# Performance work log

Hardware: AMD Instinct MI355X
Metric: run time of the kernel (lower is better)

Reference implementation:

```python
import jax, jax.numpy as jnp
import numpy as np

N = 50000      # num_nodes
E = 800000     # num_edges
F = 29         # num_node_features
IN = F + 3     # in_channels after hstack with pos
H = 64         # hidden_dim
B = 50         # batch_size (num graphs)
L = 7          # num GINConv layers


def setup_inputs() -> dict:
    key = jax.random.key(0)
    ks = jax.random.split(key, 12)
    s_in = 1.0 / np.sqrt(IN)
    s_h = 1.0 / np.sqrt(H)
    return {
        "x": jax.random.normal(ks[0], (N, F), jnp.float32),
        "pos": jax.random.normal(ks[1], (N, 3), jnp.float32),
        "edge_index": jax.random.randint(ks[2], (2, E), 0, N),
        "batch": jnp.sort(jax.random.randint(ks[3], (N,), 0, B)),
        # GINConv l: MLP = Linear(in,H) -> ReLU -> Linear(H,H)
        "W1_first": jax.random.normal(ks[4], (IN, H), jnp.float32) * s_in,
        "W1_rest": jax.random.normal(ks[5], (L - 1, H, H), jnp.float32) * s_h,
        "b1": jax.random.normal(ks[6], (L, H), jnp.float32) * 0.01,
        "W2": jax.random.normal(ks[7], (L, H, H), jnp.float32) * s_h,
        "b2": jax.random.normal(ks[8], (L, H), jnp.float32) * 0.01,
        "lin_w": jax.random.normal(ks[9], (H, 1), jnp.float32) * s_h,
        "lin_b": jax.random.normal(ks[10], (1,), jnp.float32) * 0.01,
    }


def reference(x, pos, edge_index, batch, W1_first, W1_rest, b1, W2, b2, lin_w, lin_b):
    src, dst = edge_index[0], edge_index[1]
    h = jnp.concatenate([x, pos], axis=1)  # [N, IN]

    def gin_conv(h, Wa, ba, Wb, bb):
        # sum aggregation of source features at destination nodes, eps=0
        agg = jax.ops.segment_sum(h[src], dst, num_segments=N)
        z = h + agg
        z = jax.nn.relu(z @ Wa + ba)
        return z @ Wb + bb

    h = jax.nn.relu(gin_conv(h, W1_first, b1[0], W2[0], b2[0]))
    for l in range(1, L):
        h = gin_conv(h, W1_rest[l - 1], b1[l], W2[l], b2[l])
        if l < L - 1:  # no activation after last conv (jk=None)
            h = jax.nn.relu(h)

    # global mean pool per graph
    sums = jax.ops.segment_sum(h, batch, num_segments=B)            # [B, H]
    counts = jax.ops.segment_sum(jnp.ones((N,), h.dtype), batch, num_segments=B)
    pooled = sums / jnp.maximum(counts, 1.0)[:, None]

    return pooled @ lin_w + lin_b  # [B, 1]
```

## Files before the change

kernel.cpp:

```cpp
#include <hip/hip_runtime.h>
#include <stdint.h>

#define NF 29
#define HD 64
#define NL 7
#define LDW 72
#define NCHUNK 256
#define BSH 8
#define PER_M (64 * LDW)

typedef __attribute__((ext_vector_type(8))) __bf16 bf16x8;
typedef __attribute__((ext_vector_type(4))) float floatx4;

__device__ __forceinline__ unsigned short f2bf(float x) {
    unsigned u = __float_as_uint(x);
    unsigned r = (u + 0x7fffu + ((u >> 16) & 1u)) >> 16;
    return (unsigned short)r;
}
__device__ __forceinline__ unsigned pack_bf2(float x, float y) {
    return (unsigned)f2bf(x) | ((unsigned)f2bf(y) << 16);
}
__device__ __forceinline__ float bflo(uint32_t u) { return __uint_as_float(u << 16); }
__device__ __forceinline__ float bfhi(uint32_t u) { return __uint_as_float(u & 0xffff0000u); }

__global__ void init_kernel(const float* __restrict__ x, const float* __restrict__ pos,
                            unsigned short* __restrict__ h0,
                            const float* __restrict__ W1f, const float* __restrict__ W1r,
                            const float* __restrict__ W2, unsigned short* __restrict__ wpk,
                            int N) {
    int t = blockIdx.x * blockDim.x + threadIdx.x;
    if (t < NL * 2 * PER_M) {
        int l = t / (2 * PER_M);
        int r = t - l * 2 * PER_M;
        int m = r / PER_M;
        int q = r - m * PER_M;
        int j = q / LDW, k = q - j * LDW;
        float v = 0.f;
        if (m == 0) {
            int ind = (l == 0) ? 32 : 64;
            if (k < ind) v = (l == 0) ? W1f[k * 64 + j]
                                      : W1r[(size_t)(l - 1) * 4096 + (size_t)k * 64 + j];
        } else {
            if (k < 64) v = W2[(size_t)l * 4096 + (size_t)k * 64 + j];
        }
        wpk[t] = f2bf(v);
    }
    if (t < N * 32) {
        int n = t >> 5, f = t & 31;
        float v = (f < NF) ? x[n * NF + f] : pos[n * 3 + (f - NF)];
        h0[t] = f2bf(v);
    }
}

__global__ void bucket_hist_kernel(const int* __restrict__ dst, int E, int chunk,
                                   int* __restrict__ bcnt, int* __restrict__ bsum) {
    __shared__ int hist[256];
    int tid = threadIdx.x;
    hist[tid] = 0;
    __syncthreads();
    int lo = blockIdx.x * chunk, hi = min(E, lo + chunk);
    for (int e = lo + tid; e < hi; e += 256) atomicAdd(&hist[dst[e] >> BSH], 1);
    __syncthreads();
    bcnt[tid * NCHUNK + blockIdx.x] = hist[tid];
    if (hist[tid]) atomicAdd(&bsum[tid], hist[tid]);
}

__global__ void bstart_scan_kernel(const int* __restrict__ bsum, int* __restrict__ bstart,
                                   int* __restrict__ rowptr, int nbuk, int N, int E) {
    __shared__ int s[256];
    int t = threadIdx.x;
    s[t] = (t < nbuk) ? bsum[t] : 0;
    __syncthreads();
    for (int off = 1; off < 256; off <<= 1) {
        int v = (t >= off) ? s[t - off] : 0;
        __syncthreads();
        s[t] += v;
        __syncthreads();
    }
    bstart[t] = (t == 0) ? 0 : s[t - 1];
    if (t == 255) bstart[256] = s[255];
    if (t == 0) rowptr[N] = E;
}

__global__ void bucket_off_kernel(const int* __restrict__ bcnt, const int* __restrict__ bstart,
                                  int* __restrict__ boffT) {
    __shared__ int s[256];
    int b = blockIdx.x, t = threadIdx.x;
    int c = bcnt[b * NCHUNK + t];
    s[t] = c;
    __syncthreads();
    for (int off = 1; off < 256; off <<= 1) {
        int v = (t >= off) ? s[t - off] : 0;
        __syncthreads();
        s[t] += v;
        __syncthreads();
    }
    int excl = s[t] - c;
    boffT[t * 256 + b] = bstart[b] + excl;
}

__global__ void bucket_scatter_kernel(const int* __restrict__ src, const int* __restrict__ dst,
                                      int E, int chunk, const int* __restrict__ boffT,
                                      unsigned int* __restrict__ ebuf) {
    __shared__ int cur[256];
    int tid = threadIdx.x, c = blockIdx.x;
    cur[tid] = boffT[c * 256 + tid];
    __syncthreads();
    int lo = c * chunk, hi = min(E, lo + chunk);
    for (int e = lo + tid; e < hi; e += 256) {
        int d = dst[e];
        int p = atomicAdd(&cur[d >> BSH], 1);
        ebuf[p] = (unsigned int)src[e] | ((unsigned int)(d & 255) << 16);
    }
}

__global__ void final_scatter_kernel(const unsigned int* __restrict__ ebuf,
                                     const int* __restrict__ bstart,
                                     int* __restrict__ rowptr,
                                     unsigned short* __restrict__ colsrc, int N) {
    __shared__ int cnt[256];
    __shared__ int cur[256];
    __shared__ int s[256];
    int b = blockIdx.x, t = threadIdx.x;
    cnt[t] = 0;
    __syncthreads();
    int lo = bstart[b], hi = bstart[b + 1];
    for (int e = lo + t; e < hi; e += 256) atomicAdd(&cnt[ebuf[e] >> 16], 1);
    __syncthreads();
    int c = cnt[t];
    s[t] = c;
    __syncthreads();
    for (int off = 1; off < 256; off <<= 1) {
        int v = (t >= off) ? s[t - off] : 0;
        __syncthreads();
        s[t] += v;
        __syncthreads();
    }
    int base = lo + s[t] - c;
    int node = (b << BSH) + t;
    if (node < N) rowptr[node] = base;
    cur[t] = base;
    __syncthreads();
    for (int e = lo + t; e < hi; e += 256) {
        unsigned int ed = ebuf[e];
        int p = atomicAdd(&cur[ed >> 16], 1);
        colsrc[p] = (unsigned short)(ed & 0xffffu);
    }
}

template<int IND, bool RELU_OUT>
__global__ __launch_bounds__(512, 8)
void gin_layer_kernel(const unsigned short* __restrict__ hin,
                      const int* __restrict__ rowptr, const unsigned short* __restrict__ colsrc,
                      const unsigned short* __restrict__ wAT, const unsigned short* __restrict__ wBT,
                      const float* __restrict__ ba, const float* __restrict__ bb,
                      unsigned short* __restrict__ hout, int N)
{
    __shared__ __align__(16) unsigned short zbuf[64 * LDW];
    __shared__ __align__(16) unsigned short t1buf[64 * LDW];

    const int tid = threadIdx.x;
    const int lane = tid & 63;
    const int w = tid >> 6;
    const int tile0 = blockIdx.x * 64;

    const uint4* hin4 = (const uint4*)hin;
    const int g = lane >> 3;
    const int j = lane & 7;
    const int node = tile0 + w * 8 + g;

    int rp;
    {
        int idx = tile0 + w * 8 + (lane < 9 ? lane : 8);
        if (idx > N) idx = N;
        rp = rowptr[idx];
    }
    int e0 = __shfl(rp, g);
    int e1 = __shfl(rp, g + 1);
    if (node >= N) { e0 = 0; e1 = 0; }

    float acc[8] = {0.f, 0.f, 0.f, 0.f, 0.f, 0.f, 0.f, 0.f};
    auto addrow = [&](uint4 u) {
        acc[0] += bflo(u.x); acc[1] += bfhi(u.x);
        acc[2] += bflo(u.y); acc[3] += bfhi(u.y);
        acc[4] += bflo(u.z); acc[5] += bfhi(u.z);
        acc[6] += bflo(u.w); acc[7] += bfhi(u.w);
    };

    if constexpr (IND == 64) {
        const int f4 = lane & 7;
        if (node < N) addrow(hin4[(size_t)node * 8 + f4]);
        int e = e0;
        int idxv = (e + j < e1) ? (int)colsrc[e + j] : 0;
        for (; e + 7 < e1; e += 8) {
            int en = e + 8;
            int idx_next = (en + j < e1) ? (int)colsrc[en + j] : 0;
            int s[8];
            #pragma unroll
            for (int q = 0; q < 8; ++q) s[q] = __shfl(idxv, g * 8 + q);
            uint4 u[8];
            #pragma unroll
            for (int q = 0; q < 8; ++q) u[q] = hin4[(size_t)s[q] * 8 + f4];
            #pragma unroll
            for (int q = 0; q < 8; ++q) addrow(u[q]);
            idxv = idx_next;
        }
        {
            int rem = e1 - e;
            #pragma unroll
            for (int q = 0; q < 8; ++q) {
                if (q < rem) {
                    int s = __shfl(idxv, g * 8 + q);
                    addrow(hin4[(size_t)s * 8 + f4]);
                }
            }
        }
        uint4 pk;
        pk.x = pack_bf2(acc[0], acc[1]); pk.y = pack_bf2(acc[2], acc[3]);
        pk.z = pack_bf2(acc[4], acc[5]); pk.w = pack_bf2(acc[6], acc[7]);
        *(uint4*)&zbuf[(w * 8 + g) * LDW + f4 * 8] = pk;
    } else {
        const int p = (lane >> 2) & 1;
        const int f4 = lane & 3;
        if (node < N && p == 0) addrow(hin4[(size_t)node * 4 + f4]);
        int e = e0 + p;
        for (; e + 7 < e1; e += 8) {
            int s0 = colsrc[e], s1 = colsrc[e + 2], s2 = colsrc[e + 4], s3 = colsrc[e + 6];
            uint4 u0 = hin4[(size_t)s0 * 4 + f4];
            uint4 u1 = hin4[(size_t)s1 * 4 + f4];
            uint4 u2 = hin4[(size_t)s2 * 4 + f4];
            uint4 u3 = hin4[(size_t)s3 * 4 + f4];
            addrow(u0); addrow(u1); addrow(u2); addrow(u3);
        }
        while (e < e1) { addrow(hin4[(size_t)colsrc[e] * 4 + f4]); e += 2; }
        #pragma unroll
        for (int i = 0; i < 8; ++i) acc[i] += __shfl_xor(acc[i], 4);
        if (p == 0) {
            uint4 pk;
            pk.x = pack_bf2(acc[0], acc[1]); pk.y = pack_bf2(acc[2], acc[3]);
            pk.z = pack_bf2(acc[4], acc[5]); pk.w = pack_bf2(acc[6], acc[7]);
            *(uint4*)&zbuf[(w * 8 + g) * LDW + f4 * 8] = pk;
        }
    }
    __syncthreads();

    const int n0 = lane & 15, quad = lane >> 4;
    const int stripe = w & 3, jhalf = w >> 2;
    const int row0 = stripe * 16;
    const int jt0 = jhalf * 2, jt1 = jhalf * 2 + 1;

    floatx4 c0, c1;
    {
        float b0v = ba[jt0 * 16 + n0], b1v = ba[jt1 * 16 + n0];
        c0 = (floatx4){b0v, b0v, b0v, b0v};
        c1 = (floatx4){b1v, b1v, b1v, b1v};
    }
    #pragma unroll
    for (int kk = 0; kk < IND / 32; ++kk) {
        bf16x8 a   = *(const bf16x8*)&zbuf[(row0 + n0) * LDW + kk * 32 + quad * 8];
        bf16x8 br0 = *(const bf16x8*)&wAT[(jt0 * 16 + n0) * LDW + kk * 32 + quad * 8];
        bf16x8 br1 = *(const bf16x8*)&wAT[(jt1 * 16 + n0) * LDW + kk * 32 + quad * 8];
        c0 = __builtin_amdgcn_mfma_f32_16x16x32_bf16(a, br0, c0, 0, 0, 0);
        c1 = __builtin_amdgcn_mfma_f32_16x16x32_bf16(a, br1, c1, 0, 0, 0);
    }
    #pragma unroll
    for (int r = 0; r < 4; ++r) {
        int row = row0 + quad * 4 + r;
        t1buf[row * LDW + jt0 * 16 + n0] = f2bf(fmaxf(c0[r], 0.f));
        t1buf[row * LDW + jt1 * 16 + n0] = f2bf(fmaxf(c1[r], 0.f));
    }
    __syncthreads();

    {
        float b0v = bb[jt0 * 16 + n0], b1v = bb[jt1 * 16 + n0];
        c0 = (floatx4){b0v, b0v, b0v, b0v};
        c1 = (floatx4){b1v, b1v, b1v, b1v};
    }
    #pragma unroll
    for (int kk = 0; kk < 2; ++kk) {
        bf16x8 a   = *(const bf16x8*)&t1buf[(row0 + n0) * LDW + kk * 32 + quad * 8];
        bf16x8 br0 = *(const bf16x8*)&wBT[(jt0 * 16 + n0) * LDW + kk * 32 + quad * 8];
        bf16x8 br1 = *(const bf16x8*)&wBT[(jt1 * 16 + n0) * LDW + kk * 32 + quad * 8];
        c0 = __builtin_amdgcn_mfma_f32_16x16x32_bf16(a, br0, c0, 0, 0, 0);
        c1 = __builtin_amdgcn_mfma_f32_16x16x32_bf16(a, br1, c1, 0, 0, 0);
    }
    #pragma unroll
    for (int r = 0; r < 4; ++r) {
        int row = row0 + quad * 4 + r;
        float v0 = c0[r], v1 = c1[r];
        if (RELU_OUT) { v0 = fmaxf(v0, 0.f); v1 = fmaxf(v1, 0.f); }
        zbuf[row * LDW + jt0 * 16 + n0] = f2bf(v0);
        zbuf[row * LDW + jt1 * 16 + n0] = f2bf(v1);
    }
    __syncthreads();

    {
        int nl = tid >> 3, c4 = tid & 7;
        int nodeo = tile0 + nl;
        if (nodeo < N) {
            uint4 v = *(const uint4*)&zbuf[nl * LDW + c4 * 8];
            ((uint4*)hout)[(size_t)nodeo * 8 + c4] = v;
        }
    }
}

__global__ void pool_kernel(const unsigned short* __restrict__ h, const int* __restrict__ batch,
                            float* __restrict__ pool, float* __restrict__ cnt, int N) {
    int lane = threadIdx.x;
    int nblk = gridDim.x;
    int per = (N + nblk - 1) / nblk;
    int lo = blockIdx.x * per, hi = min(N, lo + per);
    if (lo >= hi) return;
    int cur = batch[lo];
    float acc = 0.f, c = 0.f;
    for (int n = lo; n < hi; ++n) {
        int b = batch[n];
        if (b != cur) {
            atomicAdd(&pool[cur * HD + lane], acc);
            if (lane == 0) atomicAdd(&cnt[cur], c);
            acc = 0.f; c = 0.f; cur = b;
        }
        acc += __uint_as_float((uint32_t)h[(size_t)n * HD + lane] << 16);
        c += 1.f;
    }
    atomicAdd(&pool[cur * HD + lane], acc);
    if (lane == 0) atomicAdd(&cnt[cur], c);
}

__global__ void final_kernel(const float* __restrict__ pool, const float* __restrict__ cnt,
                             const float* __restrict__ lin_w, const float* __restrict__ lin_b,
                             float* __restrict__ out, int B) {
    int b = blockIdx.x;
    int lane = threadIdx.x;
    float c = fmaxf(cnt[b], 1.f);
    float v = pool[b * HD + lane] / c * lin_w[lane];
    for (int off = 32; off > 0; off >>= 1) v += __shfl_down(v, off);
    if (lane == 0) out[b] = v + lin_b[0];
}

extern "C" void kernel_launch(void* const* d_in, const int* in_sizes, int n_in,
                              void* d_out, int out_size, void* d_ws, size_t ws_size,
                              hipStream_t stream)
{
    const float* x   = (const float*)d_in[0];
    const float* pos = (const float*)d_in[1];
    const int*  eidx = (const int*)d_in[2];
    const int* batch = (const int*)d_in[3];
    const float* W1f = (const float*)d_in[4];
    const float* W1r = (const float*)d_in[5];
    const float* b1  = (const float*)d_in[6];
    const float* W2  = (const float*)d_in[7];
    const float* b2  = (const float*)d_in[8];
    const float* lw  = (const float*)d_in[9];
    const float* lb  = (const float*)d_in[10];

    int N = in_sizes[3];
    int E = in_sizes[2] / 2;
    int B = out_size;
    const int* src = eidx;
    const int* dst = eidx + E;

    char* ws = (char*)d_ws;
    size_t off = 0;
    auto alloc = [&](size_t bytes) -> void* {
        void* p = ws + off;
        off += (bytes + 255) & ~(size_t)255;
        return p;
    };
    unsigned short* bufA = (unsigned short*)alloc((size_t)N * HD * 2);
    unsigned short* bufB = (unsigned short*)alloc((size_t)N * HD * 2);
    int*   rowptr = (int*)  alloc((size_t)(N + 1) * 4);
    unsigned short* colsrc = (unsigned short*)alloc((size_t)E * 2);
    unsigned int* ebuf = (unsigned int*)alloc((size_t)E * 4);
    float* pool   = (float*)alloc((size_t)B * HD * 4);
    float* cnt    = (float*)alloc((size_t)B * 4);
    int*   bcnt   = (int*)  alloc((size_t)256 * NCHUNK * 4);
    int*   boffT  = (int*)  alloc((size_t)NCHUNK * 256 * 4);
    int*   bsum   = (int*)  alloc(256 * 4);
    int*   bstart = (int*)  alloc(257 * 4);
    unsigned short* wpk = (unsigned short*)alloc((size_t)NL * 2 * PER_M * 2);

    hipMemsetAsync(bsum, 0, 256 * 4, stream);
    hipMemsetAsync(pool, 0, (size_t)B * HD * 4, stream);
    hipMemsetAsync(cnt, 0, (size_t)B * 4, stream);

    int nbuk = (N + 255) >> BSH;
    int chunk = (E + NCHUNK - 1) / NCHUNK;

    init_kernel<<<(N * 32 + 255) / 256, 256, 0, stream>>>(x, pos, bufA, W1f, W1r, W2, wpk, N);
    bucket_hist_kernel<<<NCHUNK, 256, 0, stream>>>(dst, E, chunk, bcnt, bsum);
    bstart_scan_kernel<<<1, 256, 0, stream>>>(bsum, bstart, rowptr, nbuk, N, E);
    bucket_off_kernel<<<nbuk, 256, 0, stream>>>(bcnt, bstart, boffT);
    bucket_scatter_kernel<<<NCHUNK, 256, 0, stream>>>(src, dst, E, chunk, boffT, ebuf);
    final_scatter_kernel<<<nbuk, 256, 0, stream>>>(ebuf, bstart, rowptr, colsrc, N);

    const int gblocks = (N + 63) / 64;
    gin_layer_kernel<32, true><<<gblocks, 512, 0, stream>>>(
        bufA, rowptr, colsrc, wpk + 0 * PER_M, wpk + 1 * PER_M, b1, b2, bufB, N);
    unsigned short* cur_in = bufB;
    unsigned short* cur_out = bufA;
    for (int l = 1; l < NL; ++l) {
        const unsigned short* wa = wpk + (size_t)(2 * l + 0) * PER_M;
        const unsigned short* wb = wpk + (size_t)(2 * l + 1) * PER_M;
        const float* ba = b1 + l * HD;
        const float* bb = b2 + l * HD;
        if (l < NL - 1)
            gin_layer_kernel<HD, true><<<gblocks, 512, 0, stream>>>(
                cur_in, rowptr, colsrc, wa, wb, ba, bb, cur_out, N);
        else
            gin_layer_kernel<HD, false><<<gblocks, 512, 0, stream>>>(
                cur_in, rowptr, colsrc, wa, wb, ba, bb, cur_out, N);
        unsigned short* tmp = cur_in; cur_in = cur_out; cur_out = tmp;
    }
    pool_kernel<<<512, 64, 0, stream>>>(cur_in, batch, pool, cnt, N);
    final_kernel<<<B, 64, 0, stream>>>(pool, cnt, lw, lb, (float*)d_out, B);
}
```

Baseline: 291.8 us.

## Split 64-wide node features into two 32-wide halves gathered in separate passes

Stores hidden features as two separate 32-column bf16 tables. Each layer now runs a gather kernel for the low half into a staging buffer, then the fused layer kernel gathers the high half and does the MLP. The aim is to shrink each random-gather working set (1.6MB per half) so it fits better in cache and gets higher hit rates. In exchange it adds an extra kernel launch per layer, a round trip of the low-half aggregate through global memory, and a second walk of the edge list.

Measured after the change: 322.4 us. +10.5%, slower.

```diff
diff --git a/kernel.cpp b/kernel.cpp
--- a/kernel.cpp
+++ b/kernel.cpp
@@ -148,98 +148,116 @@
     }
 }
 
-template<int IND, bool RELU_OUT>
-__global__ __launch_bounds__(512, 8)
-void gin_layer_kernel(const unsigned short* __restrict__ hin,
-                      const int* __restrict__ rowptr, const unsigned short* __restrict__ colsrc,
-                      const unsigned short* __restrict__ wAT, const unsigned short* __restrict__ wBT,
-                      const float* __restrict__ ba, const float* __restrict__ bb,
-                      unsigned short* __restrict__ hout, int N)
-{
-    __shared__ __align__(16) unsigned short zbuf[64 * LDW];
-    __shared__ __align__(16) unsigned short t1buf[64 * LDW];
-
-    const int tid = threadIdx.x;
-    const int lane = tid & 63;
-    const int w = tid >> 6;
-    const int tile0 = blockIdx.x * 64;
-
-    const uint4* hin4 = (const uint4*)hin;
-    const int g = lane >> 3;
-    const int j = lane & 7;
-    const int node = tile0 + w * 8 + g;
-
-    int rp;
-    {
-        int idx = tile0 + w * 8 + (lane < 9 ? lane : 8);
-        if (idx > N) idx = N;
-        rp = rowptr[idx];
-    }
-    int e0 = __shfl(rp, g);
-    int e1 = __shfl(rp, g + 1);
-    if (node >= N) { e0 = 0; e1 = 0; }
-
-    float acc[8] = {0.f, 0.f, 0.f, 0.f, 0.f, 0.f, 0.f, 0.f};
+template<bool SELF>
+__device__ __forceinline__ void gather32(const uint4* __restrict__ tab4,
+                                         const unsigned short* __restrict__ colsrc,
+                                         int node, int e0, int e1, int lane,
+                                         float acc[8]) {
+    const int p = (lane >> 2) & 1;
+    const int f4 = lane & 3;
     auto addrow = [&](uint4 u) {
         acc[0] += bflo(u.x); acc[1] += bfhi(u.x);
         acc[2] += bflo(u.y); acc[3] += bfhi(u.y);
         acc[4] += bflo(u.z); acc[5] += bfhi(u.z);
         acc[6] += bflo(u.w); acc[7] += bfhi(u.w);
     };
-
-    if constexpr (IND == 64) {
-        const int f4 = lane & 7;
-        if (node < N) addrow(hin4[(size_t)node * 8 + f4]);
-        int e = e0;
-        int idxv = (e + j < e1) ? (int)colsrc[e + j] : 0;
-        for (; e + 7 < e1; e += 8) {
-            int en = e + 8;
-            int idx_next = (en + j < e1) ? (int)colsrc[en + j] : 0;
-            int s[8];
-            #pragma unroll
-            for (int q = 0; q < 8; ++q) s[q] = __shfl(idxv, g * 8 + q);
-            uint4 u[8];
-            #pragma unroll
-            for (int q = 0; q < 8; ++q) u[q] = hin4[(size_t)s[q] * 8 + f4];
-            #pragma unroll
-            for (int q = 0; q < 8; ++q) addrow(u[q]);
-            idxv = idx_next;
-        }
-        {
-            int rem = e1 - e;
-            #pragma unroll
-            for (int q = 0; q < 8; ++q) {
-                if (q < rem) {
-                    int s = __shfl(idxv, g * 8 + q);
-                    addrow(hin4[(size_t)s * 8 + f4]);
-                }
-            }
-        }
+    if (SELF && node >= 0 && p == 0) addrow(tab4[(size_t)node * 4 + f4]);
+    int e = e0 + p;
+    for (; e + 7 < e1; e += 8) {
+        int s0 = colsrc[e], s1 = colsrc[e + 2], s2 = colsrc[e + 4], s3 = colsrc[e + 6];
+        uint4 u0 = tab4[(size_t)s0 * 4 + f4];
+        uint4 u1 = tab4[(size_t)s1 * 4 + f4];
+        uint4 u2 = tab4[(size_t)s2 * 4 + f4];
+        uint4 u3 = tab4[(size_t)s3 * 4 + f4];
+        addrow(u0); addrow(u1); addrow(u2); addrow(u3);
+    }
+    while (e < e1) { addrow(tab4[(size_t)colsrc[e] * 4 + f4]); e += 2; }
+    #pragma unroll
+    for (int i = 0; i < 8; ++i) acc[i] += __shfl_xor(acc[i], 4);
+}
+
+__global__ __launch_bounds__(512, 8)
+void gather_lo_kernel(const unsigned short* __restrict__ hA,
+                      const int* __restrict__ rowptr, const unsigned short* __restrict__ colsrc,
+                      unsigned short* __restrict__ zlo, int N)
+{
+    const int tid = threadIdx.x;
+    const int lane = tid & 63;
+    const int w = tid >> 6;
+    const int tile0 = blockIdx.x * 64;
+    const int g = lane >> 3;
+    const int node = tile0 + w * 8 + g;
+
+    int rp;
+    {
+        int idx = tile0 + w * 8 + (lane < 9 ? lane : 8);
+        if (idx > N) idx = N;
+        rp = rowptr[idx];
+    }
+    int e0 = __shfl(rp, g);
+    int e1 = __shfl(rp, g + 1);
+    bool valid = (node < N);
+    if (!valid) { e0 = 0; e1 = 0; }
+
+    float acc[8] = {0.f, 0.f, 0.f, 0.f, 0.f, 0.f, 0.f, 0.f};
+    gather32<true>((const uint4*)hA, colsrc, valid ? node : -1, e0, e1, lane, acc);
+
+    if (valid && ((lane >> 2) & 1) == 0) {
         uint4 pk;
         pk.x = pack_bf2(acc[0], acc[1]); pk.y = pack_bf2(acc[2], acc[3]);
         pk.z = pack_bf2(acc[4], acc[5]); pk.w = pack_bf2(acc[6], acc[7]);
-        *(uint4*)&zbuf[(w * 8 + g) * LDW + f4 * 8] = pk;
-    } else {
-        const int p = (lane >> 2) & 1;
-        const int f4 = lane & 3;
-        if (node < N && p == 0) addrow(hin4[(size_t)node * 4 + f4]);
-        int e = e0 + p;
-        for (; e + 7 < e1; e += 8) {
-            int s0 = colsrc[e], s1 = colsrc[e + 2], s2 = colsrc[e + 4], s3 = colsrc[e + 6];
-            uint4 u0 = hin4[(size_t)s0 * 4 + f4];
-            uint4 u1 = hin4[(size_t)s1 * 4 + f4];
-            uint4 u2 = hin4[(size_t)s2 * 4 + f4];
-            uint4 u3 = hin4[(size_t)s3 * 4 + f4];
-            addrow(u0); addrow(u1); addrow(u2); addrow(u3);
-        }
-        while (e < e1) { addrow(hin4[(size_t)colsrc[e] * 4 + f4]); e += 2; }
-        #pragma unroll
-        for (int i = 0; i < 8; ++i) acc[i] += __shfl_xor(acc[i], 4);
-        if (p == 0) {
+        ((uint4*)zlo)[(size_t)node * 4 + (lane & 3)] = pk;
+    }
+}
+
+template<bool FIRST, bool RELU_OUT>
+__global__ __launch_bounds__(512, 8)
+void gin_layer_kernel(const unsigned short* __restrict__ table32,
+                      const unsigned short* __restrict__ zlo,
+                      const int* __restrict__ rowptr, const unsigned short* __restrict__ colsrc,
+                      const unsigned short* __restrict__ wAT, const unsigned short* __restrict__ wBT,
+                      const float* __restrict__ ba, const float* __restrict__ bb,
+                      unsigned short* __restrict__ hA_out, unsigned short* __restrict__ hB_out,
+                      int N)
+{
+    __shared__ __align__(16) unsigned short zbuf[64 * LDW];
+    __shared__ __align__(16) unsigned short t1buf[64 * LDW];
+
+    const int tid = threadIdx.x;
+    const int lane = tid & 63;
+    const int w = tid >> 6;
+    const int tile0 = blockIdx.x * 64;
+    const int g = lane >> 3;
+    const int node = tile0 + w * 8 + g;
+
+    if constexpr (!FIRST) {
+        if (tid < 256) {
+            int nl = tid >> 2, c4 = tid & 3;
+            *(uint4*)&zbuf[nl * LDW + c4 * 8] = ((const uint4*)zlo)[(size_t)(tile0 + nl) * 4 + c4];
+        }
+    }
+
+    {
+        int rp;
+        {
+            int idx = tile0 + w * 8 + (lane < 9 ? lane : 8);
+            if (idx > N) idx = N;
+            rp = rowptr[idx];
+        }
+        int e0 = __shfl(rp, g);
+        int e1 = __shfl(rp, g + 1);
+        bool valid = (node < N);
+        if (!valid) { e0 = 0; e1 = 0; }
+
+        float acc[8] = {0.f, 0.f, 0.f, 0.f, 0.f, 0.f, 0.f, 0.f};
+        gather32<true>((const uint4*)table32, colsrc, valid ? node : -1, e0, e1, lane, acc);
+
+        constexpr int ZOFF = FIRST ? 0 : 32;
+        if (((lane >> 2) & 1) == 0) {
             uint4 pk;
             pk.x = pack_bf2(acc[0], acc[1]); pk.y = pack_bf2(acc[2], acc[3]);
             pk.z = pack_bf2(acc[4], acc[5]); pk.w = pack_bf2(acc[6], acc[7]);
-            *(uint4*)&zbuf[(w * 8 + g) * LDW + f4 * 8] = pk;
+            *(uint4*)&zbuf[(w * 8 + g) * LDW + ZOFF + (lane & 3) * 8] = pk;
         }
     }
     __syncthreads();
@@ -248,6 +266,7 @@
     const int stripe = w & 3, jhalf = w >> 2;
     const int row0 = stripe * 16;
     const int jt0 = jhalf * 2, jt1 = jhalf * 2 + 1;
+    constexpr int KK1 = FIRST ? 1 : 2;
 
     floatx4 c0, c1;
     {
@@ -256,7 +275,7 @@
         c1 = (floatx4){b1v, b1v, b1v, b1v};
     }
     #pragma unroll
-    for (int kk = 0; kk < IND / 32; ++kk) {
+    for (int kk = 0; kk < KK1; ++kk) {
         bf16x8 a   = *(const bf16x8*)&zbuf[(row0 + n0) * LDW + kk * 32 + quad * 8];
         bf16x8 br0 = *(const bf16x8*)&wAT[(jt0 * 16 + n0) * LDW + kk * 32 + quad * 8];
         bf16x8 br1 = *(const bf16x8*)&wAT[(jt1 * 16 + n0) * LDW + kk * 32 + quad * 8];
@@ -299,18 +318,23 @@
         int nodeo = tile0 + nl;
         if (nodeo < N) {
             uint4 v = *(const uint4*)&zbuf[nl * LDW + c4 * 8];
-            ((uint4*)hout)[(size_t)nodeo * 8 + c4] = v;
-        }
-    }
-}
-
-__global__ void pool_kernel(const unsigned short* __restrict__ h, const int* __restrict__ batch,
+            if (c4 < 4) ((uint4*)hA_out)[(size_t)nodeo * 4 + c4] = v;
+            else        ((uint4*)hB_out)[(size_t)nodeo * 4 + (c4 - 4)] = v;
+        }
+    }
+}
+
+__global__ void pool_kernel(const unsigned short* __restrict__ hA,
+                            const unsigned short* __restrict__ hB,
+                            const int* __restrict__ batch,
                             float* __restrict__ pool, float* __restrict__ cnt, int N) {
     int lane = threadIdx.x;
     int nblk = gridDim.x;
     int per = (N + nblk - 1) / nblk;
     int lo = blockIdx.x * per, hi = min(N, lo + per);
     if (lo >= hi) return;
+    const unsigned short* tab = (lane < 32) ? hA : hB;
+    int f = lane & 31;
     int cur = batch[lo];
     float acc = 0.f, c = 0.f;
     for (int n = lo; n < hi; ++n) {
@@ -320,7 +344,7 @@
             if (lane == 0) atomicAdd(&cnt[cur], c);
             acc = 0.f; c = 0.f; cur = b;
         }
-        acc += __uint_as_float((uint32_t)h[(size_t)n * HD + lane] << 16);
+        acc += __uint_as_float((uint32_t)tab[(size_t)n * 32 + f] << 16);
         c += 1.f;
     }
     atomicAdd(&pool[cur * HD + lane], acc);
@@ -359,6 +383,7 @@
     int B = out_size;
     const int* src = eidx;
     const int* dst = eidx + E;
+    int Npad = N + 64;
 
     char* ws = (char*)d_ws;
     size_t off = 0;
@@ -367,8 +392,12 @@
         off += (bytes + 255) & ~(size_t)255;
         return p;
     };
-    unsigned short* bufA = (unsigned short*)alloc((size_t)N * HD * 2);
-    unsigned short* bufB = (unsigned short*)alloc((size_t)N * HD * 2);
+    unsigned short* h0tab = (unsigned short*)alloc((size_t)Npad * 32 * 2);
+    unsigned short* hA0 = (unsigned short*)alloc((size_t)Npad * 32 * 2);
+    unsigned short* hB0 = (unsigned short*)alloc((size_t)Npad * 32 * 2);
+    unsigned short* hA1 = (unsigned short*)alloc((size_t)Npad * 32 * 2);
+    unsigned short* hB1 = (unsigned short*)alloc((size_t)Npad * 32 * 2);
+    unsigned short* zlo = (unsigned short*)alloc((size_t)Npad * 32 * 2);
     int*   rowptr = (int*)  alloc((size_t)(N + 1) * 4);
     unsigned short* colsrc = (unsigned short*)alloc((size_t)E * 2);
     unsigned int* ebuf = (unsigned int*)alloc((size_t)E * 4);
@@ -387,7 +416,7 @@
     int nbuk = (N + 255) >> BSH;
     int chunk = (E + NCHUNK - 1) / NCHUNK;
 
-    init_kernel<<<(N * 32 + 255) / 256, 256, 0, stream>>>(x, pos, bufA, W1f, W1r, W2, wpk, N);
+    init_kernel<<<(N * 32 + 255) / 256, 256, 0, stream>>>(x, pos, h0tab, W1f, W1r, W2, wpk, N);
     bucket_hist_kernel<<<NCHUNK, 256, 0, stream>>>(dst, E, chunk, bcnt, bsum);
     bstart_scan_kernel<<<1, 256, 0, stream>>>(bsum, bstart, rowptr, nbuk, N, E);
     bucket_off_kernel<<<nbuk, 256, 0, stream>>>(bcnt, bstart, boffT);
@@ -395,23 +424,29 @@
     final_scatter_kernel<<<nbuk, 256, 0, stream>>>(ebuf, bstart, rowptr, colsrc, N);
 
     const int gblocks = (N + 63) / 64;
-    gin_layer_kernel<32, true><<<gblocks, 512, 0, stream>>>(
-        bufA, rowptr, colsrc, wpk + 0 * PER_M, wpk + 1 * PER_M, b1, b2, bufB, N);
-    unsigned short* cur_in = bufB;
-    unsigned short* cur_out = bufA;
+
+    gin_layer_kernel<true, true><<<gblocks, 512, 0, stream>>>(
+        h0tab, nullptr, rowptr, colsrc, wpk + 0 * PER_M, wpk + 1 * PER_M,
+        b1, b2, hA1, hB1, N);
+
+    unsigned short* curA = hA1; unsigned short* curB = hB1;
+    unsigned short* nxtA = hA0; unsigned short* nxtB = hB0;
     for (int l = 1; l < NL; ++l) {
         const unsigned short* wa = wpk + (size_t)(2 * l + 0) * PER_M;
         const unsigned short* wb = wpk + (size_t)(2 * l + 1) * PER_M;
         const float* ba = b1 + l * HD;
         const float* bb = b2 + l * HD;
+        gather_lo_kernel<<<gblocks, 512, 0, stream>>>(curA, rowptr, colsrc, zlo, N);
         if (l < NL - 1)
-            gin_layer_kernel<HD, true><<<gblocks, 512, 0, stream>>>(
-                cur_in, rowptr, colsrc, wa, wb, ba, bb, cur_out, N);
+            gin_layer_kernel<false, true><<<gblocks, 512, 0, stream>>>(
+                curB, zlo, rowptr, colsrc, wa, wb, ba, bb, nxtA, nxtB, N);
         else
-            gin_layer_kernel<HD, false><<<gblocks, 512, 0, stream>>>(
-                cur_in, rowptr, colsrc, wa, wb, ba, bb, cur_out, N);
-        unsigned short* tmp = cur_in; cur_in = cur_out; cur_out = tmp;
-    }
-    pool_kernel<<<512, 64, 0, stream>>>(cur_in, batch, pool, cnt, N);
+            gin_layer_kernel<false, false><<<gblocks, 512, 0, stream>>>(
+                curB, zlo, rowptr, colsrc, wa, wb, ba, bb, nxtA, nxtB, N);
+        unsigned short* t;
+        t = curA; curA = nxtA; nxtA = t;
+        t = curB; curB = nxtB; nxtB = t;
+    }
+    pool_kernel<<<512, 64, 0, stream>>>(curA, curB, batch, pool, cnt, N);
     final_kernel<<<B, 64, 0, stream>>>(pool, cnt, lw, lb, (float*)d_out, B);
 }
```
